# Performance work log

Hardware: AMD Instinct MI355X
Metric: run time of the kernel (lower is better)

The kernel has to match this reference:

```python
import jax, jax.numpy as jnp
import numpy as np

STRIDE = 1
PADDING = 1

def setup_inputs() -> dict:
    key = jax.random.key(0)
    k1, k2, k3 = jax.random.split(key, 3)
    x = jax.random.normal(k1, (32, 64, 112, 112), dtype=jnp.float32)
    weight = jax.random.normal(k2, (128, 64, 3, 3), dtype=jnp.float32)
    bias = jax.random.normal(k3, (128,), dtype=jnp.float32)
    return {"x": x, "weight": weight, "bias": bias}

def reference(x, weight, bias):
    # Equivalent of the explicit-loop conv: standard cross-correlation conv2d
    # x: [N, C, H, W], weight: [O, C, KH, KW] -> out: [N, O, OH, OW]
    out = jax.lax.conv_general_dilated(
        x, weight,
        window_strides=(STRIDE, STRIDE),
        padding=[(PADDING, PADDING), (PADDING, PADDING)],
        dimension_numbers=("NCHW", "OIHW", "NCHW"),
    )
    return out + bias[None, :, None, None]
```

## Files before the change

kernel.cpp:

```cpp
#include <hip/hip_runtime.h>

#define CIN 64
#define OC 128
#define HW 112
#define HWHW (HW*HW)
#define NIMG 32

#define XN_ELEMS (NIMG*HWHW*CIN)
#define WT_OFF_EL (XN_ELEMS + 128)

#define ROWE (114*64)

typedef __attribute__((ext_vector_type(8))) short short8;
typedef __attribute__((ext_vector_type(4))) float floatx4;

__device__ inline unsigned short f2bf(float f) {
    unsigned u = __float_as_uint(f);
    u += 0x7fffu + ((u >> 16) & 1u);
    return (unsigned short)(u >> 16);
}

__device__ inline void async16(const unsigned short* g, unsigned short* l) {
    __builtin_amdgcn_global_load_lds(
        (const __attribute__((address_space(1))) void*)g,
        (__attribute__((address_space(3))) void*)l, 16, 0, 0);
}

__global__ __launch_bounds__(256) void xform_x(const float* __restrict__ x,
                                               unsigned short* __restrict__ xws)
{
    __shared__ float s[HW * (CIN + 1)];
    const int tid = threadIdx.x;
    const int n = blockIdx.x / HW;
    const int h = blockIdx.x % HW;

    const float* xp = x + (size_t)n * CIN * HWHW + h * HW;
    for (int idx = tid; idx < CIN * HW; idx += 256) {
        int c = idx / HW;
        int w = idx - c * HW;
        s[w * (CIN + 1) + c] = xp[c * HWHW + w];
    }
    __syncthreads();

    unsigned short* op = xws + ((size_t)(n * HW + h)) * HW * CIN;
    for (int idx = tid; idx < (CIN * HW) / 8; idx += 256) {
        int w  = idx >> 3;
        int c0 = (idx & 7) * 8;
        union { unsigned short us[8]; uint4 v; } u;
        #pragma unroll
        for (int j = 0; j < 8; ++j)
            u.us[j] = f2bf(s[w * (CIN + 1) + c0 + j]);
        *(uint4*)(op + w * CIN + c0) = u.v;
    }
}

__global__ __launch_bounds__(256) void xform_w(const float* __restrict__ wgt,
                                               unsigned short* __restrict__ ws16)
{
    const int idx = blockIdx.x * 256 + threadIdx.x;
    const int c = idx & 63;
    const int o = (idx >> 6) & 127;
    const int t = idx >> 13;
    const float v = wgt[(o * CIN + c) * 9 + t];
    ws16[WT_OFF_EL + ((size_t)(t * 2 + (c >> 5)) * 128 + o) * 32 + (c & 31)] = f2bf(v);
}

__global__ __launch_bounds__(256, 2) void conv_mfma(
    const unsigned short* __restrict__ ws16,
    const float* __restrict__ bias,
    float* __restrict__ out)
{
    __shared__ unsigned short sx[4 * ROWE];

    const int tid  = threadIdx.x;
    const int wave = tid >> 6;
    const int lane = tid & 63;
    const int lane_lo = lane & 15;
    const int lane_hi = lane >> 4;

    const int bid0 = blockIdx.x;
    const int bid  = (bid0 & 7) * 224 + (bid0 >> 3);
    const int n   = bid / 56;
    const int rp  = bid % 56;
    const int h0  = rp * 2;

    {
        const int slot = wave;
        const int hr = h0 + slot - 1;
        unsigned short* rowb = sx + slot * ROWE;
        if ((unsigned)hr < (unsigned)HW) {
            if (lane < 8)        *(uint4*)(rowb + lane * 8) = (uint4){0,0,0,0};
            else if (lane < 16)  *(uint4*)(rowb + 113*64 + (lane - 8) * 8) = (uint4){0,0,0,0};
            const unsigned short* gr = ws16 + ((size_t)(n * HW + hr)) * HW * CIN;
            const int grp = lane >> 3;
            const int sub = lane & 7;
            const int swz = sub ^ ((1 + grp) & 7);
            const unsigned short* gl = gr + grp * 64 + swz * 8;
            #pragma unroll
            for (int j = 0; j < 14; ++j)
                async16(gl + j * 512, rowb + (1 + j * 8) * 64);
        } else {
            #pragma unroll
            for (int t = 0; t < 14; ++t)
                *(uint4*)(rowb + t * 512 + lane * 8) = (uint4){0,0,0,0};
            if (lane < 16) *(uint4*)(rowb + 7168 + lane * 8) = (uint4){0,0,0,0};
        }
    }
    __syncthreads();

    floatx4 acc[7][4];
    #pragma unroll
    for (int mt = 0; mt < 7; ++mt)
        #pragma unroll
        for (int ot = 0; ot < 4; ++ot)
            acc[mt][ot] = (floatx4){0.f, 0.f, 0.f, 0.f};

    const unsigned short* wA = ws16 + WT_OFF_EL;
    const int row_idx = wave >> 1;
    const int o0 = (wave & 1) * 64;
    const int aL = (o0 + lane_lo) * 32 + lane_hi * 8;

    short8 a[2][2][4];
    #pragma unroll
    for (int k01 = 0; k01 < 2; ++k01)
        #pragma unroll
        for (int ot = 0; ot < 4; ++ot)
            a[0][k01][ot] = *(const short8*)(wA + k01 * 4096 + ot * 512 + aL);

    #pragma unroll
    for (int tap = 0; tap < 9; ++tap) {
        const int dh = tap / 3 - 1;
        const int dw = tap % 3 - 1;
        const int cur = tap & 1, nxt = cur ^ 1;
        if (tap < 8) {
            #pragma unroll
            for (int k01 = 0; k01 < 2; ++k01)
                #pragma unroll
                for (int ot = 0; ot < 4; ++ot)
                    a[nxt][k01][ot] = *(const short8*)(
                        wA + ((tap + 1) * 2 + k01) * 4096 + ot * 512 + aL);
        }
        const int colL = lane_lo + dw + 1;
        const unsigned short* sb = sx + (row_idx + 1 + dh) * ROWE + colL * 64;
        const int sw0 = (lane_hi ^ (colL & 7)) * 8;
        const int sw1 = ((lane_hi + 4) ^ (colL & 7)) * 8;

        #pragma unroll
        for (int mt = 0; mt < 7; ++mt) {
            const short8 b0 = *(const short8*)(sb + mt * 1024 + sw0);
            const short8 b1 = *(const short8*)(sb + mt * 1024 + sw1);
            #pragma unroll
            for (int ot = 0; ot < 4; ++ot)
                acc[mt][ot] = __builtin_amdgcn_mfma_f32_16x16x32_bf16(
                    a[cur][0][ot], b0, acc[mt][ot], 0, 0, 0);
            #pragma unroll
            for (int ot = 0; ot < 4; ++ot)
                acc[mt][ot] = __builtin_amdgcn_mfma_f32_16x16x32_bf16(
                    a[cur][1][ot], b1, acc[mt][ot], 0, 0, 0);
        }
    }

    const int h = h0 + row_idx;
    #pragma unroll
    for (int ot = 0; ot < 4; ++ot) {
        const int ob = o0 + ot * 16 + lane_hi * 4;
        const float4 bv = *(const float4*)(bias + ob);
        #pragma unroll
        for (int mt = 0; mt < 7; ++mt) {
            const int w = mt * 16 + lane_lo;
            float* op = out + ((size_t)(n * OC + ob) * HW + h) * HW + w;
            op[0]        = acc[mt][ot].x + bv.x;
            op[HWHW]     = acc[mt][ot].y + bv.y;
            op[2 * HWHW] = acc[mt][ot].z + bv.z;
            op[3 * HWHW] = acc[mt][ot].w + bv.w;
        }
    }
}

extern "C" void kernel_launch(void* const* d_in, const int* in_sizes, int n_in,
                              void* d_out, int out_size, void* d_ws, size_t ws_size,
                              hipStream_t stream) {
    const float* x    = (const float*)d_in[0];
    const float* wgt  = (const float*)d_in[1];
    const float* bias = (const float*)d_in[2];
    float* out = (float*)d_out;
    unsigned short* ws16 = (unsigned short*)d_ws;

    hipLaunchKernelGGL(xform_x, dim3(NIMG * HW), dim3(256), 0, stream, x, ws16);
    hipLaunchKernelGGL(xform_w, dim3(288), dim3(256), 0, stream, wgt, ws16);
    hipLaunchKernelGGL(conv_mfma, dim3(NIMG * 56), dim3(256), 0, stream,
                       ws16, bias, out);
}
```

Measured before the change: 330.8 us.

## Fuse NCHW-to-NHWC bf16 input transform into conv kernel tile load

Removes the separate xform_x pass that wrote a bf16 NHWC copy of the input to workspace. The conv kernel now reads fp32 NCHW rows directly, converts channel pairs to packed bf16 with v_cvt_pk_bf16_f32, and writes them into the swizzled LDS layout. This avoids a full write and reread of the transformed activation tensor and one kernel launch. In exchange, each input row is loaded and converted up to twice by neighbouring row-pair blocks, and the async global-to-LDS loads are replaced by synchronous strided fp32 loads and scattered 4-byte LDS stores.

```diff
diff --git a/kernel.cpp b/kernel.cpp
--- a/kernel.cpp
+++ b/kernel.cpp
@@ -6,8 +6,6 @@
 #define HWHW (HW*HW)
 #define NIMG 32
 
-#define XN_ELEMS (NIMG*HWHW*CIN)
-#define WT_OFF_EL (XN_ELEMS + 128)
 
 #define ROWE (114*64)
 
@@ -20,40 +18,6 @@
     return (unsigned short)(u >> 16);
 }
 
-__device__ inline void async16(const unsigned short* g, unsigned short* l) {
-    __builtin_amdgcn_global_load_lds(
-        (const __attribute__((address_space(1))) void*)g,
-        (__attribute__((address_space(3))) void*)l, 16, 0, 0);
-}
-
-__global__ __launch_bounds__(256) void xform_x(const float* __restrict__ x,
-                                               unsigned short* __restrict__ xws)
-{
-    __shared__ float s[HW * (CIN + 1)];
-    const int tid = threadIdx.x;
-    const int n = blockIdx.x / HW;
-    const int h = blockIdx.x % HW;
-
-    const float* xp = x + (size_t)n * CIN * HWHW + h * HW;
-    for (int idx = tid; idx < CIN * HW; idx += 256) {
-        int c = idx / HW;
-        int w = idx - c * HW;
-        s[w * (CIN + 1) + c] = xp[c * HWHW + w];
-    }
-    __syncthreads();
-
-    unsigned short* op = xws + ((size_t)(n * HW + h)) * HW * CIN;
-    for (int idx = tid; idx < (CIN * HW) / 8; idx += 256) {
-        int w  = idx >> 3;
-        int c0 = (idx & 7) * 8;
-        union { unsigned short us[8]; uint4 v; } u;
-        #pragma unroll
-        for (int j = 0; j < 8; ++j)
-            u.us[j] = f2bf(s[w * (CIN + 1) + c0 + j]);
-        *(uint4*)(op + w * CIN + c0) = u.v;
-    }
-}
-
 __global__ __launch_bounds__(256) void xform_w(const float* __restrict__ wgt,
                                                unsigned short* __restrict__ ws16)
 {
@@ -62,11 +26,12 @@
     const int o = (idx >> 6) & 127;
     const int t = idx >> 13;
     const float v = wgt[(o * CIN + c) * 9 + t];
-    ws16[WT_OFF_EL + ((size_t)(t * 2 + (c >> 5)) * 128 + o) * 32 + (c & 31)] = f2bf(v);
+    ws16[((size_t)(t * 2 + (c >> 5)) * 128 + o) * 32 + (c & 31)] = f2bf(v);
 }
 
-__global__ __launch_bounds__(256, 2) void conv_mfma(
-    const unsigned short* __restrict__ ws16,
+__global__ __launch_bounds__(256, 2) void conv_fused(
+    const float* __restrict__ x,
+    const unsigned short* __restrict__ wgt16,
     const float* __restrict__ bias,
     float* __restrict__ out)
 {
@@ -85,25 +50,45 @@
     const int h0  = rp * 2;
 
     {
-        const int slot = wave;
-        const int hr = h0 + slot - 1;
-        unsigned short* rowb = sx + slot * ROWE;
-        if ((unsigned)hr < (unsigned)HW) {
-            if (lane < 8)        *(uint4*)(rowb + lane * 8) = (uint4){0,0,0,0};
-            else if (lane < 16)  *(uint4*)(rowb + 113*64 + (lane - 8) * 8) = (uint4){0,0,0,0};
-            const unsigned short* gr = ws16 + ((size_t)(n * HW + hr)) * HW * CIN;
-            const int grp = lane >> 3;
-            const int sub = lane & 7;
-            const int swz = sub ^ ((1 + grp) & 7);
-            const unsigned short* gl = gr + grp * 64 + swz * 8;
-            #pragma unroll
-            for (int j = 0; j < 14; ++j)
-                async16(gl + j * 512, rowb + (1 + j * 8) * 64);
-        } else {
-            #pragma unroll
-            for (int t = 0; t < 14; ++t)
-                *(uint4*)(rowb + t * 512 + lane * 8) = (uint4){0,0,0,0};
-            if (lane < 16) *(uint4*)(rowb + 7168 + lane * 8) = (uint4){0,0,0,0};
+        const int p    = tid & 31;
+        const int g    = tid >> 5;
+        const int c    = p * 2;
+        const int cblk = p >> 2;
+        const int crem = c & 7;
+        #pragma unroll 1
+        for (int s = 0; s < 4; ++s) {
+            const int hr = h0 + s - 1;
+            unsigned short* rowb = sx + s * ROWE;
+            if ((unsigned)hr < (unsigned)HW) {
+                const float* xr = x + ((size_t)(n * CIN + c)) * HWHW + hr * HW;
+                #pragma unroll
+                for (int k = 0; k < 4; ++k) {
+                    const int q = g + 8 * k;
+                    if (q < 28) {
+                        const float4 fa = *(const float4*)(xr + 4 * q);
+                        const float4 fb = *(const float4*)(xr + HWHW + 4 * q);
+                        #pragma unroll
+                        for (int j = 0; j < 4; ++j) {
+                            const int col = 4 * q + j + 1;
+                            const float sa = ((const float*)&fa)[j];
+                            const float sb = ((const float*)&fb)[j];
+                            unsigned d;
+                            asm("v_cvt_pk_bf16_f32 %0, %1, %2"
+                                : "=v"(d) : "v"(sa), "v"(sb));
+                            *(unsigned*)(rowb + col * 64 +
+                                         ((cblk ^ (col & 7)) << 3) + crem) = d;
+                        }
+                    }
+                }
+                if (tid < 8)       *(uint4*)(rowb + tid * 8) = (uint4){0,0,0,0};
+                else if (tid < 16) *(uint4*)(rowb + 113*64 + (tid - 8) * 8) = (uint4){0,0,0,0};
+            } else {
+                #pragma unroll
+                for (int k = 0; k < 4; ++k) {
+                    const int e = tid + k * 256;
+                    if (e < ROWE / 8) *(uint4*)(rowb + e * 8) = (uint4){0,0,0,0};
+                }
+            }
         }
     }
     __syncthreads();
@@ -115,7 +100,7 @@
         for (int ot = 0; ot < 4; ++ot)
             acc[mt][ot] = (floatx4){0.f, 0.f, 0.f, 0.f};
 
-    const unsigned short* wA = ws16 + WT_OFF_EL;
+    const unsigned short* wA = wgt16;
     const int row_idx = wave >> 1;
     const int o0 = (wave & 1) * 64;
     const int aL = (o0 + lane_lo) * 32 + lane_hi * 8;
@@ -186,8 +171,7 @@
     float* out = (float*)d_out;
     unsigned short* ws16 = (unsigned short*)d_ws;
 
-    hipLaunchKernelGGL(xform_x, dim3(NIMG * HW), dim3(256), 0, stream, x, ws16);
     hipLaunchKernelGGL(xform_w, dim3(288), dim3(256), 0, stream, wgt, ws16);
-    hipLaunchKernelGGL(conv_mfma, dim3(NIMG * 56), dim3(256), 0, stream,
-                       ws16, bias, out);
+    hipLaunchKernelGGL(conv_fused, dim3(NIMG * 56), dim3(256), 0, stream,
+                       x, ws16, bias, out);
 }
```

New measurement: 339.3 us. 1.03x slower.

## Stage input rows with hand-counted vmcnt waits to overlap loads with MFMA taps

Applied to the files above, without the earlier changes.

Splits each halo row load across all four waves and issues the weight loads for the first three taps before the input rows. Hand-written s_waitcnt vmcnt thresholds plus barriers let compute start once the first needed rows have landed, instead of waiting for everything. Later rows arrive while the first taps run, and weights are now triple-buffered with a two-tap prefetch distance. The risk is fragile counter arithmetic: if the compiler emits vector memory ops in a different order or count, the data can race, and the extra weight registers may hurt occupancy.

```diff
diff --git a/kernel.cpp b/kernel.cpp
--- a/kernel.cpp
+++ b/kernel.cpp
@@ -13,6 +13,12 @@
 
 typedef __attribute__((ext_vector_type(8))) short short8;
 typedef __attribute__((ext_vector_type(4))) float floatx4;
+
+#define WAIT_V8  asm volatile("s_waitcnt vmcnt(8) lgkmcnt(0)" ::: "memory")
+#define WAIT_V6  asm volatile("s_waitcnt vmcnt(6) lgkmcnt(0)" ::: "memory")
+#define WAIT_V0  asm volatile("s_waitcnt vmcnt(0) lgkmcnt(0)" ::: "memory")
+#define WAIT_V19 asm volatile("s_waitcnt vmcnt(19)" ::: "memory")
+#define WAIT_V40 asm volatile("s_waitcnt vmcnt(40)" ::: "memory")
 
 __device__ inline unsigned short f2bf(float f) {
     unsigned u = __float_as_uint(f);
@@ -83,62 +89,88 @@
     const int n   = bid / 56;
     const int rp  = bid % 56;
     const int h0  = rp * 2;
-
-    {
-        const int slot = wave;
-        const int hr = h0 + slot - 1;
-        unsigned short* rowb = sx + slot * ROWE;
-        if ((unsigned)hr < (unsigned)HW) {
-            if (lane < 8)        *(uint4*)(rowb + lane * 8) = (uint4){0,0,0,0};
-            else if (lane < 16)  *(uint4*)(rowb + 113*64 + (lane - 8) * 8) = (uint4){0,0,0,0};
-            const unsigned short* gr = ws16 + ((size_t)(n * HW + hr)) * HW * CIN;
-            const int grp = lane >> 3;
-            const int sub = lane & 7;
-            const int swz = sub ^ ((1 + grp) & 7);
-            const unsigned short* gl = gr + grp * 64 + swz * 8;
-            #pragma unroll
-            for (int j = 0; j < 14; ++j)
-                async16(gl + j * 512, rowb + (1 + j * 8) * 64);
-        } else {
-            #pragma unroll
-            for (int t = 0; t < 14; ++t)
-                *(uint4*)(rowb + t * 512 + lane * 8) = (uint4){0,0,0,0};
-            if (lane < 16) *(uint4*)(rowb + 7168 + lane * 8) = (uint4){0,0,0,0};
-        }
-    }
-    __syncthreads();
-
-    floatx4 acc[7][4];
-    #pragma unroll
-    for (int mt = 0; mt < 7; ++mt)
-        #pragma unroll
-        for (int ot = 0; ot < 4; ++ot)
-            acc[mt][ot] = (floatx4){0.f, 0.f, 0.f, 0.f};
+    const bool interior = (rp > 0) && (rp < 55);
 
     const unsigned short* wA = ws16 + WT_OFF_EL;
     const int row_idx = wave >> 1;
     const int o0 = (wave & 1) * 64;
     const int aL = (o0 + lane_lo) * 32 + lane_hi * 8;
 
-    short8 a[2][2][4];
-    #pragma unroll
-    for (int k01 = 0; k01 < 2; ++k01)
+    short8 a[3][2][4];
+    #pragma unroll
+    for (int t = 0; t < 3; ++t)
+        #pragma unroll
+        for (int k01 = 0; k01 < 2; ++k01)
+            #pragma unroll
+            for (int ot = 0; ot < 4; ++ot)
+                a[t][k01][ot] = *(const short8*)(
+                    wA + (t * 2 + k01) * 4096 + ot * 512 + aL);
+
+    asm volatile("" ::: "memory");
+
+    {
+        const int grp = lane >> 3;
+        const int sub = lane & 7;
+        const int swz = sub ^ ((1 + grp) & 7);
+        #pragma unroll
+        for (int s = 0; s < 4; ++s) {
+            const int hr = h0 + s - 1;
+            unsigned short* rowb = sx + s * ROWE;
+            if ((unsigned)hr < (unsigned)HW) {
+                const unsigned short* gl = ws16 +
+                    ((size_t)(n * HW + hr)) * HW * CIN + grp * 64 + swz * 8;
+                #pragma unroll
+                for (int k = 0; k < 4; ++k) {
+                    const int j = wave + 4 * k;
+                    if (j < 14) async16(gl + j * 512, rowb + (1 + j * 8) * 64);
+                }
+            } else {
+                #pragma unroll
+                for (int k = 0; k < 4; ++k) {
+                    const int j = wave + 4 * k;
+                    if (j < 14)
+                        *(uint4*)(rowb + (1 + j * 8) * 64 + lane * 8) = (uint4){0,0,0,0};
+                }
+            }
+        }
+        unsigned short* rowb = sx + wave * ROWE;
+        if (lane < 8)       *(uint4*)(rowb + lane * 8) = (uint4){0,0,0,0};
+        else if (lane < 16) *(uint4*)(rowb + 113*64 + (lane - 8) * 8) = (uint4){0,0,0,0};
+    }
+
+    if (interior) { if (wave < 2) { WAIT_V8; } else { WAIT_V6; } }
+    else          { WAIT_V0; }
+    __builtin_amdgcn_s_barrier();
+    __builtin_amdgcn_sched_barrier(0);
+
+    floatx4 acc[7][4];
+    #pragma unroll
+    for (int mt = 0; mt < 7; ++mt)
         #pragma unroll
         for (int ot = 0; ot < 4; ++ot)
-            a[0][k01][ot] = *(const short8*)(wA + k01 * 4096 + ot * 512 + aL);
+            acc[mt][ot] = (floatx4){0.f, 0.f, 0.f, 0.f};
 
     #pragma unroll
     for (int tap = 0; tap < 9; ++tap) {
+        if (tap == 3) {
+            if (interior) { WAIT_V19; } else { WAIT_V0; }
+            __builtin_amdgcn_s_barrier();
+            __builtin_amdgcn_sched_barrier(0);
+        }
+        if (tap == 6) {
+            if (interior) { WAIT_V40; } else { WAIT_V0; }
+            __builtin_amdgcn_s_barrier();
+            __builtin_amdgcn_sched_barrier(0);
+        }
         const int dh = tap / 3 - 1;
         const int dw = tap % 3 - 1;
-        const int cur = tap & 1, nxt = cur ^ 1;
-        if (tap < 8) {
+        if (tap >= 1 && tap <= 6) {
             #pragma unroll
             for (int k01 = 0; k01 < 2; ++k01)
                 #pragma unroll
                 for (int ot = 0; ot < 4; ++ot)
-                    a[nxt][k01][ot] = *(const short8*)(
-                        wA + ((tap + 1) * 2 + k01) * 4096 + ot * 512 + aL);
+                    a[(tap + 2) % 3][k01][ot] = *(const short8*)(
+                        wA + ((tap + 2) * 2 + k01) * 4096 + ot * 512 + aL);
         }
         const int colL = lane_lo + dw + 1;
         const unsigned short* sb = sx + (row_idx + 1 + dh) * ROWE + colL * 64;
@@ -152,11 +184,11 @@
             #pragma unroll
             for (int ot = 0; ot < 4; ++ot)
                 acc[mt][ot] = __builtin_amdgcn_mfma_f32_16x16x32_bf16(
-                    a[cur][0][ot], b0, acc[mt][ot], 0, 0, 0);
+                    a[tap % 3][0][ot], b0, acc[mt][ot], 0, 0, 0);
             #pragma unroll
             for (int ot = 0; ot < 4; ++ot)
                 acc[mt][ot] = __builtin_amdgcn_mfma_f32_16x16x32_bf16(
-                    a[cur][1][ot], b1, acc[mt][ot], 0, 0, 0);
+                    a[tap % 3][1][ot], b1, acc[mt][ot], 0, 0, 0);
         }
     }
 
```

New measurement: 336.2 us. No clear change (+1.6%).
